# Performance work log

Measured on AMD Instinct MI355X. Metric: run time of the kernel, lower is better.

The kernel has to match this reference:

```python
import jax, jax.numpy as jnp
import numpy as np

N, C, E = 10000, 128, 640000  # nodes, channels, edges


def setup_inputs() -> dict:
    key = jax.random.key(0)
    k1, k2, k3, k4 = jax.random.split(key, 4)
    x = jax.random.normal(k1, (N, C), dtype=jnp.float32)
    src = jax.random.randint(k2, (E,), 0, N)  # source node of each edge (neighbor j)
    dst = jax.random.randint(k3, (E,), 0, N)  # destination node (center i)
    # EdgeConv linear: in = 2*C (concat[x_i, x_j - x_i]), out = C
    W = jax.random.normal(k4, (2 * C, C), dtype=jnp.float32) / np.sqrt(2.0 * C)
    b = jnp.zeros((C,), dtype=jnp.float32)
    return {"x": x, "W": W, "b": b, "src": src, "dst": dst}


def reference(x, W, b, src, dst):
    # EdgeConv: h_i = max_{j in N(i)} Linear([x_i, x_j - x_i]); then ReLU
    xi = x[dst]                                   # [E, C] gather center feats
    xj = x[src]                                   # [E, C] gather neighbor feats
    msg = jnp.concatenate([xi, xj - xi], axis=-1) @ W + b   # [E, C]
    agg = jax.ops.segment_max(msg, dst, num_segments=x.shape[0])  # [N, C]
    # nodes with no incoming edges get -inf from segment_max; zero them
    agg = jnp.where(jnp.isfinite(agg), agg, jnp.zeros_like(agg))
    return jax.nn.relu(agg)
```

## Files before the change

### kernel.cpp

```cpp
#include <hip/hip_runtime.h>
#include <cstdint>


#define C_CH 128
#define NBLK 128
#define NMAX_LDS 10016

typedef __attribute__((ext_vector_type(8))) short bf16x8;
typedef __attribute__((ext_vector_type(4))) float f32x4;
typedef __attribute__((ext_vector_type(4))) unsigned int u32x4;

static inline size_t align_up(size_t v, size_t a) { return (v + a - 1) & ~(a - 1); }

__device__ inline unsigned f2bf_bits(float f) {
    unsigned u = __builtin_bit_cast(unsigned, f);
    return (u + 0x7FFFu + ((u >> 16) & 1u)) >> 16;
}

__global__ __launch_bounds__(256) void gemm_mfma(const float* __restrict__ x,
                                                 const float* __restrict__ W,
                                                 const float* __restrict__ bias,
                                                 float* __restrict__ Aarr,
                                                 unsigned short* __restrict__ Bbf,
                                                 int Nn) {
    __shared__ unsigned short Wh[64][136];
    __shared__ unsigned short Wl[64][136];
    int tid = threadIdx.x;
    int col0 = blockIdx.y * 64;
    bool isA = (col0 < C_CH);
    for (int idx = tid; idx < 64 * 64; idx += 256) {
        int c = idx & 63, k = (idx >> 6) * 2;
        int gc = col0 + c;
        float w0, w1;
        if (isA) {
            w0 = W[k * C_CH + gc] - W[(k + C_CH) * C_CH + gc];
            w1 = W[(k + 1) * C_CH + gc] - W[(k + 1 + C_CH) * C_CH + gc];
        } else {
            int g2 = gc - C_CH;
            w0 = W[(k + C_CH) * C_CH + g2];
            w1 = W[(k + 1 + C_CH) * C_CH + g2];
        }
        unsigned h0 = f2bf_bits(w0), h1 = f2bf_bits(w1);
        float hf0 = __builtin_bit_cast(float, h0 << 16);
        float hf1 = __builtin_bit_cast(float, h1 << 16);
        unsigned l0 = f2bf_bits(w0 - hf0), l1 = f2bf_bits(w1 - hf1);
        *(unsigned*)&Wh[c][k] = h0 | (h1 << 16);
        *(unsigned*)&Wl[c][k] = l0 | (l1 << 16);
    }
    __syncthreads();
    int lane = tid & 63, wv = tid >> 6;
    int r0 = blockIdx.x * 64 + wv * 16;
    int arow = min(r0 + (lane & 15), Nn - 1);
    int kgrp = (lane >> 4) * 8;
    f32x4 acc[4] = {};
#pragma unroll
    for (int kk = 0; kk < 4; ++kk) {
        int k0 = kk * 32 + kgrp;
        const float* xp = &x[(size_t)arow * C_CH + k0];
        float4 v0 = *(const float4*)xp;
        float4 v1 = *(const float4*)(xp + 4);
        float vv[8] = {v0.x, v0.y, v0.z, v0.w, v1.x, v1.y, v1.z, v1.w};
        bf16x8 ah, al;
#pragma unroll
        for (int u = 0; u < 8; ++u) {
            unsigned hb = f2bf_bits(vv[u]);
            float hf = __builtin_bit_cast(float, hb << 16);
            ah[u] = (short)hb;
            al[u] = (short)f2bf_bits(vv[u] - hf);
        }
#pragma unroll
        for (int j = 0; j < 4; ++j) {
            int c = j * 16 + (lane & 15);
            bf16x8 bh = *(const bf16x8*)&Wh[c][k0];
            bf16x8 bl = *(const bf16x8*)&Wl[c][k0];
            acc[j] = __builtin_amdgcn_mfma_f32_16x16x32_bf16(ah, bh, acc[j], 0, 0, 0);
            acc[j] = __builtin_amdgcn_mfma_f32_16x16x32_bf16(al, bh, acc[j], 0, 0, 0);
            acc[j] = __builtin_amdgcn_mfma_f32_16x16x32_bf16(ah, bl, acc[j], 0, 0, 0);
        }
    }
#pragma unroll
    for (int j = 0; j < 4; ++j) {
        int gc = col0 + j * 16 + (lane & 15);
        float badd = isA ? bias[gc] : 0.f;
#pragma unroll
        for (int reg = 0; reg < 4; ++reg) {
            int row = r0 + (lane >> 4) * 4 + reg;
            if (row < Nn) {
                if (isA) Aarr[(size_t)row * C_CH + gc] = acc[j][reg] + badd;
                else     Bbf[(size_t)row * C_CH + (gc - C_CH)] =
                             (unsigned short)f2bf_bits(acc[j][reg]);
            }
        }
    }
}

__global__ __launch_bounds__(256) void hist_k(const int* __restrict__ dst,
                                              int* __restrict__ T,
                                              int E_, int Nn, int chunk) {
    __shared__ int ldeg[NMAX_LDS];
    int tid = threadIdx.x, b = blockIdx.x;
    for (int i = tid; i < Nn; i += 256) ldeg[i] = 0;
    __syncthreads();
    int e0 = b * chunk, e1 = min(e0 + chunk, E_);
    int n4 = (e1 - e0) >> 2;
    const int4* d4p = (const int4*)(dst + e0);
    for (int i = tid; i < n4; i += 256) {
        int4 d = d4p[i];
        atomicAdd(&ldeg[d.x], 1); atomicAdd(&ldeg[d.y], 1);
        atomicAdd(&ldeg[d.z], 1); atomicAdd(&ldeg[d.w], 1);
    }
    for (int i = e0 + n4 * 4 + tid; i < e1; i += 256) atomicAdd(&ldeg[dst[i]], 1);
    __syncthreads();
    int* Tb = T + (size_t)b * Nn;
    for (int i = tid; i < Nn; i += 256) Tb[i] = ldeg[i];
}

__global__ __launch_bounds__(256) void colscan_k(int* __restrict__ T,
                                                 int* __restrict__ deg, int Nn) {
    int tid = threadIdx.x;
    int lane = tid & 63;
    int n = blockIdx.x * 4 + (tid >> 6);
    if (n >= Nn) return;
    size_t st = (size_t)Nn;
    int e0 = T[lane * st + n];
    int e1 = T[(lane + 64) * st + n];
    int i0 = e0, i1 = e1;
#pragma unroll
    for (int off = 1; off < 64; off <<= 1) {
        int t0 = __shfl_up(i0, off);
        int t1 = __shfl_up(i1, off);
        if (lane >= off) { i0 += t0; i1 += t1; }
    }
    int tot0 = __shfl(i0, 63);
    int tot1 = __shfl(i1, 63);
    T[lane * st + n] = i0 - e0;
    T[(lane + 64) * st + n] = tot0 + i1 - e1;
    if (lane == 0) deg[n] = tot0 + tot1;
}

__global__ __launch_bounds__(1024) void scan_k(const int* __restrict__ deg,
                                               int* __restrict__ offs, int n) {
    __shared__ int wsum[16];
    const int PER = 16;
    int tid = threadIdx.x;
    int base = tid * PER;
    int s = 0;
#pragma unroll
    for (int k = 0; k < PER; ++k) {
        int idx = base + k;
        s += (idx < n) ? deg[idx] : 0;
    }
    int lane = tid & 63, wid = tid >> 6;
    int pref = s;
#pragma unroll
    for (int off = 1; off < 64; off <<= 1) {
        int t = __shfl_up(pref, off);
        if (lane >= off) pref += t;
    }
    if (lane == 63) wsum[wid] = pref;
    __syncthreads();
    if (tid < 16) {
        int v = wsum[tid];
#pragma unroll
        for (int off = 1; off < 16; off <<= 1) {
            int t = __shfl_up(v, off, 16);
            if (tid >= off) v += t;
        }
        wsum[tid] = v;
    }
    __syncthreads();
    int run = ((wid > 0) ? wsum[wid - 1] : 0) + (pref - s);
#pragma unroll
    for (int k = 0; k < PER; ++k) {
        int idx = base + k;
        int v = (idx < n) ? deg[idx] : 0;
        if (idx < n) offs[idx] = run;
        run += v;
    }
    if (tid == 1023) offs[n] = run;
}

__global__ __launch_bounds__(256) void scatter_k(const int* __restrict__ src,
                                                 const int* __restrict__ dst,
                                                 const int* __restrict__ T,
                                                 const int* __restrict__ offs,
                                                 int* __restrict__ ssrc,
                                                 int E_, int Nn, int chunk) {
    __shared__ int sbase[NMAX_LDS];
    __shared__ int ldeg[NMAX_LDS];
    int tid = threadIdx.x, b = blockIdx.x;
    const int* Tb = T + (size_t)b * Nn;
    for (int i = tid; i < Nn; i += 256) {
        sbase[i] = offs[i] + Tb[i];
        ldeg[i] = 0;
    }
    __syncthreads();
    int e0 = b * chunk, e1 = min(e0 + chunk, E_);
    int n4 = (e1 - e0) >> 2;
    const int4* d4p = (const int4*)(dst + e0);
    const int4* s4p = (const int4*)(src + e0);
    for (int i = tid; i < n4; i += 256) {
        int4 d = d4p[i];
        int4 sv = s4p[i];
        int r;
        r = atomicAdd(&ldeg[d.x], 1); ssrc[sbase[d.x] + r] = sv.x;
        r = atomicAdd(&ldeg[d.y], 1); ssrc[sbase[d.y] + r] = sv.y;
        r = atomicAdd(&ldeg[d.z], 1); ssrc[sbase[d.z] + r] = sv.z;
        r = atomicAdd(&ldeg[d.w], 1); ssrc[sbase[d.w] + r] = sv.w;
    }
    for (int i = e0 + n4 * 4 + tid; i < e1; i += 256) {
        int d = dst[i];
        int r = atomicAdd(&ldeg[d], 1);
        ssrc[sbase[d] + r] = src[i];
    }
}

__global__ __launch_bounds__(256) void node_max(const float* __restrict__ Aarr,
                                                const unsigned short* __restrict__ Bbf,
                                                const int* __restrict__ offs,
                                                const int* __restrict__ ssrc,
                                                float* __restrict__ out, int Nn) {
    int i = blockIdx.x;
    int tid = threadIdx.x;
    int s = offs[i], e = offs[i + 1];
    if (e == s) {
        if (tid < 32) ((float4*)out)[(size_t)i * 32 + tid] = make_float4(0.f, 0.f, 0.f, 0.f);
        return;
    }
    __shared__ int js[256];
    __shared__ float pm[4][16][8];
    int g = tid >> 4;
    int l16 = tid & 15;
    int cb = l16 * 8;
    float m[8];
#pragma unroll
    for (int k = 0; k < 8; ++k) m[k] = -INFINITY;
    for (int base = s; base < e; base += 256) {
        __syncthreads();
        js[tid] = ssrc[min(base + tid, e - 1)];
        __syncthreads();
        int cnt = min(256, e - base);
        for (int t = g; t < cnt; t += 64) {
            u32x4 v[4];
#pragma unroll
            for (int u = 0; u < 4; ++u) {
                int idx = min(t + 16 * u, cnt - 1);
                v[u] = *(const u32x4*)&Bbf[(size_t)js[idx] * C_CH + cb];
            }
#pragma unroll
            for (int u = 0; u < 4; ++u) {
#pragma unroll
                for (int p = 0; p < 4; ++p) {
                    unsigned w = v[u][p];
                    float f0 = __builtin_bit_cast(float, w << 16);
                    float f1 = __builtin_bit_cast(float, w & 0xFFFF0000u);
                    m[2 * p]     = fmaxf(m[2 * p], f0);
                    m[2 * p + 1] = fmaxf(m[2 * p + 1], f1);
                }
            }
        }
    }
#pragma unroll
    for (int k = 0; k < 8; ++k) {
        m[k] = fmaxf(m[k], __shfl_xor(m[k], 16));
        m[k] = fmaxf(m[k], __shfl_xor(m[k], 32));
    }
    __syncthreads();
    int wid = tid >> 6;
    if ((tid & 63) < 16) {
#pragma unroll
        for (int k = 0; k < 8; ++k) pm[wid][l16][k] = m[k];
    }
    __syncthreads();
    if (tid < C_CH) {
        int c = tid;
        float mm = fmaxf(fmaxf(pm[0][c >> 3][c & 7], pm[1][c >> 3][c & 7]),
                         fmaxf(pm[2][c >> 3][c & 7], pm[3][c >> 3][c & 7]));
        float a = Aarr[(size_t)i * C_CH + c];
        out[(size_t)i * C_CH + c] = fmaxf(a + mm, 0.f);
    }
}

extern "C" void kernel_launch(void* const* d_in, const int* in_sizes, int n_in,
                              void* d_out, int out_size, void* d_ws, size_t ws_size,
                              hipStream_t stream) {
    const float* x = (const float*)d_in[0];
    const float* W = (const float*)d_in[1];
    const float* b = (const float*)d_in[2];
    const int* src = (const int*)d_in[3];
    const int* dst = (const int*)d_in[4];
    float* out = (float*)d_out;

    const int N = in_sizes[0] / C_CH;
    const int E = in_sizes[3];
    const int chunk = (((E + NBLK - 1) / NBLK) + 3) & ~3;

    char* w = (char*)d_ws;
    float* Aarr = (float*)w;            w += align_up((size_t)N * C_CH * 4, 256);
    unsigned short* Bbf = (unsigned short*)w;  w += align_up((size_t)N * C_CH * 2, 256);
    int* deg = (int*)w;                 w += align_up((size_t)N * 4, 256);
    int* offs = (int*)w;                w += align_up((size_t)(N + 1) * 4, 256);
    int* T = (int*)w;                   w += align_up((size_t)NBLK * N * 4, 256);
    int* ssrc = (int*)w;                w += align_up((size_t)E * 4, 256);

    gemm_mfma<<<dim3((N + 63) / 64, 4), 256, 0, stream>>>(x, W, b, Aarr, Bbf, N);
    hist_k<<<NBLK, 256, 0, stream>>>(dst, T, E, N, chunk);
    colscan_k<<<(N + 3) / 4, 256, 0, stream>>>(T, deg, N);
    scan_k<<<1, 1024, 0, stream>>>(deg, offs, N);
    scatter_k<<<NBLK, 256, 0, stream>>>(src, dst, T, offs, ssrc, E, N, chunk);
    node_max<<<N, 256, 0, stream>>>(Aarr, Bbf, offs, ssrc, out, N);
}
```

Baseline: 147.5 us.

## Bucket edges by groups of 16 destinations and reduce with LDS atomicMax

Replaces the per-node CSR sort with a coarse counting sort into buckets of 16 destination nodes, storing the packed (src, local dst) pair per edge. This shrinks the histogram and scan tables (640 buckets instead of 10000 nodes) and uses 256 blocks. A new bucket_max kernel gives one 512-thread block per bucket and accumulates per-channel maxima in LDS through monotonic-key atomicMax. The cost is that each edge now reads its bf16 row with scalar 2-byte loads and does LDS atomics per channel, instead of the previous vectorised register max reduction.

```diff
diff --git a/kernel.cpp b/kernel.cpp
--- a/kernel.cpp
+++ b/kernel.cpp
@@ -3,18 +3,21 @@
 
 
 #define C_CH 128
-#define NBLK 128
-#define NMAX_LDS 10016
+#define HBLK 256
+#define BSH 4
+#define BPAD 640
 
 typedef __attribute__((ext_vector_type(8))) short bf16x8;
 typedef __attribute__((ext_vector_type(4))) float f32x4;
-typedef __attribute__((ext_vector_type(4))) unsigned int u32x4;
 
 static inline size_t align_up(size_t v, size_t a) { return (v + a - 1) & ~(a - 1); }
 
 __device__ inline unsigned f2bf_bits(float f) {
     unsigned u = __builtin_bit_cast(unsigned, f);
     return (u + 0x7FFFu + ((u >> 16) & 1u)) >> 16;
+}
+__device__ inline unsigned mono_key(unsigned u) {
+    return (u & 0x80000000u) ? ~u : (u | 0x80000000u);
 }
 
 __global__ __launch_bounds__(256) void gemm_mfma(const float* __restrict__ x,
@@ -94,48 +97,49 @@
     }
 }
 
-__global__ __launch_bounds__(256) void hist_k(const int* __restrict__ dst,
-                                              int* __restrict__ T,
-                                              int E_, int Nn, int chunk) {
-    __shared__ int ldeg[NMAX_LDS];
+__global__ __launch_bounds__(256) void hist2_k(const int* __restrict__ dst,
+                                               int* __restrict__ T2,
+                                               int E_, int NBq, int chunk) {
+    __shared__ int cnt[BPAD];
     int tid = threadIdx.x, b = blockIdx.x;
-    for (int i = tid; i < Nn; i += 256) ldeg[i] = 0;
+    for (int i = tid; i < BPAD; i += 256) cnt[i] = 0;
     __syncthreads();
     int e0 = b * chunk, e1 = min(e0 + chunk, E_);
     int n4 = (e1 - e0) >> 2;
     const int4* d4p = (const int4*)(dst + e0);
     for (int i = tid; i < n4; i += 256) {
         int4 d = d4p[i];
-        atomicAdd(&ldeg[d.x], 1); atomicAdd(&ldeg[d.y], 1);
-        atomicAdd(&ldeg[d.z], 1); atomicAdd(&ldeg[d.w], 1);
-    }
-    for (int i = e0 + n4 * 4 + tid; i < e1; i += 256) atomicAdd(&ldeg[dst[i]], 1);
-    __syncthreads();
-    int* Tb = T + (size_t)b * Nn;
-    for (int i = tid; i < Nn; i += 256) Tb[i] = ldeg[i];
-}
-
-__global__ __launch_bounds__(256) void colscan_k(int* __restrict__ T,
-                                                 int* __restrict__ deg, int Nn) {
+        atomicAdd(&cnt[d.x >> BSH], 1); atomicAdd(&cnt[d.y >> BSH], 1);
+        atomicAdd(&cnt[d.z >> BSH], 1); atomicAdd(&cnt[d.w >> BSH], 1);
+    }
+    for (int i = e0 + n4 * 4 + tid; i < e1; i += 256) atomicAdd(&cnt[dst[i] >> BSH], 1);
+    __syncthreads();
+    int* Tb = T2 + (size_t)b * BPAD;
+    for (int i = tid; i < NBq; i += 256) Tb[i] = cnt[i];
+}
+
+__global__ __launch_bounds__(256) void colscan2_k(int* __restrict__ T2,
+                                                  int* __restrict__ deg2, int NBq) {
     int tid = threadIdx.x;
     int lane = tid & 63;
-    int n = blockIdx.x * 4 + (tid >> 6);
-    if (n >= Nn) return;
-    size_t st = (size_t)Nn;
-    int e0 = T[lane * st + n];
-    int e1 = T[(lane + 64) * st + n];
-    int i0 = e0, i1 = e1;
+    int q = blockIdx.x * 4 + (tid >> 6);
+    if (q >= NBq) return;
+    int e[4], p[4];
+#pragma unroll
+    for (int k = 0; k < 4; ++k) e[k] = T2[(size_t)(lane + 64 * k) * BPAD + q];
+    int s = 0;
+#pragma unroll
+    for (int k = 0; k < 4; ++k) { p[k] = s; s += e[k]; }
+    int incl = s;
 #pragma unroll
     for (int off = 1; off < 64; off <<= 1) {
-        int t0 = __shfl_up(i0, off);
-        int t1 = __shfl_up(i1, off);
-        if (lane >= off) { i0 += t0; i1 += t1; }
-    }
-    int tot0 = __shfl(i0, 63);
-    int tot1 = __shfl(i1, 63);
-    T[lane * st + n] = i0 - e0;
-    T[(lane + 64) * st + n] = tot0 + i1 - e1;
-    if (lane == 0) deg[n] = tot0 + tot1;
+        int t = __shfl_up(incl, off);
+        if (lane >= off) incl += t;
+    }
+    int excl = incl - s;
+#pragma unroll
+    for (int k = 0; k < 4; ++k) T2[(size_t)(lane + 64 * k) * BPAD + q] = excl + p[k];
+    if (lane == 63) deg2[q] = incl;
 }
 
 __global__ __launch_bounds__(1024) void scan_k(const int* __restrict__ deg,
@@ -180,104 +184,93 @@
     if (tid == 1023) offs[n] = run;
 }
 
-__global__ __launch_bounds__(256) void scatter_k(const int* __restrict__ src,
-                                                 const int* __restrict__ dst,
-                                                 const int* __restrict__ T,
-                                                 const int* __restrict__ offs,
-                                                 int* __restrict__ ssrc,
-                                                 int E_, int Nn, int chunk) {
-    __shared__ int sbase[NMAX_LDS];
-    __shared__ int ldeg[NMAX_LDS];
+__global__ __launch_bounds__(256) void scatter2_k(const int* __restrict__ src,
+                                                  const int* __restrict__ dst,
+                                                  const int* __restrict__ T2,
+                                                  const int* __restrict__ offs2,
+                                                  unsigned* __restrict__ epack,
+                                                  int E_, int NBq, int chunk) {
+    __shared__ int sbase[BPAD];
+    __shared__ int cur[BPAD];
     int tid = threadIdx.x, b = blockIdx.x;
-    const int* Tb = T + (size_t)b * Nn;
-    for (int i = tid; i < Nn; i += 256) {
-        sbase[i] = offs[i] + Tb[i];
-        ldeg[i] = 0;
+    const int* Tb = T2 + (size_t)b * BPAD;
+    for (int i = tid; i < NBq; i += 256) {
+        sbase[i] = offs2[i] + Tb[i];
+        cur[i] = 0;
     }
     __syncthreads();
     int e0 = b * chunk, e1 = min(e0 + chunk, E_);
     int n4 = (e1 - e0) >> 2;
     const int4* d4p = (const int4*)(dst + e0);
     const int4* s4p = (const int4*)(src + e0);
+    const int LM = (1 << BSH) - 1;
     for (int i = tid; i < n4; i += 256) {
         int4 d = d4p[i];
         int4 sv = s4p[i];
-        int r;
-        r = atomicAdd(&ldeg[d.x], 1); ssrc[sbase[d.x] + r] = sv.x;
-        r = atomicAdd(&ldeg[d.y], 1); ssrc[sbase[d.y] + r] = sv.y;
-        r = atomicAdd(&ldeg[d.z], 1); ssrc[sbase[d.z] + r] = sv.z;
-        r = atomicAdd(&ldeg[d.w], 1); ssrc[sbase[d.w] + r] = sv.w;
+        int q, r;
+        q = d.x >> BSH; r = atomicAdd(&cur[q], 1);
+        epack[sbase[q] + r] = ((unsigned)sv.x << BSH) | (unsigned)(d.x & LM);
+        q = d.y >> BSH; r = atomicAdd(&cur[q], 1);
+        epack[sbase[q] + r] = ((unsigned)sv.y << BSH) | (unsigned)(d.y & LM);
+        q = d.z >> BSH; r = atomicAdd(&cur[q], 1);
+        epack[sbase[q] + r] = ((unsigned)sv.z << BSH) | (unsigned)(d.z & LM);
+        q = d.w >> BSH; r = atomicAdd(&cur[q], 1);
+        epack[sbase[q] + r] = ((unsigned)sv.w << BSH) | (unsigned)(d.w & LM);
     }
     for (int i = e0 + n4 * 4 + tid; i < e1; i += 256) {
         int d = dst[i];
-        int r = atomicAdd(&ldeg[d], 1);
-        ssrc[sbase[d] + r] = src[i];
-    }
-}
-
-__global__ __launch_bounds__(256) void node_max(const float* __restrict__ Aarr,
-                                                const unsigned short* __restrict__ Bbf,
-                                                const int* __restrict__ offs,
-                                                const int* __restrict__ ssrc,
-                                                float* __restrict__ out, int Nn) {
-    int i = blockIdx.x;
+        int q = d >> BSH;
+        int r = atomicAdd(&cur[q], 1);
+        epack[sbase[q] + r] = ((unsigned)src[i] << BSH) | (unsigned)(d & LM);
+    }
+}
+
+__global__ __launch_bounds__(512) void bucket_max(const float* __restrict__ Aarr,
+                                                  const unsigned short* __restrict__ Bbf,
+                                                  const int* __restrict__ offs2,
+                                                  const unsigned* __restrict__ epack,
+                                                  float* __restrict__ out, int Nn) {
+    int q = blockIdx.x;
+    int n0 = q << BSH;
+    if (n0 >= Nn) return;
+    __shared__ unsigned acc[1 << BSH][C_CH];
     int tid = threadIdx.x;
-    int s = offs[i], e = offs[i + 1];
-    if (e == s) {
-        if (tid < 32) ((float4*)out)[(size_t)i * 32 + tid] = make_float4(0.f, 0.f, 0.f, 0.f);
-        return;
-    }
-    __shared__ int js[256];
-    __shared__ float pm[4][16][8];
-    int g = tid >> 4;
-    int l16 = tid & 15;
-    int cb = l16 * 8;
-    float m[8];
-#pragma unroll
-    for (int k = 0; k < 8; ++k) m[k] = -INFINITY;
-    for (int base = s; base < e; base += 256) {
-        __syncthreads();
-        js[tid] = ssrc[min(base + tid, e - 1)];
-        __syncthreads();
-        int cnt = min(256, e - base);
-        for (int t = g; t < cnt; t += 64) {
-            u32x4 v[4];
-#pragma unroll
-            for (int u = 0; u < 4; ++u) {
-                int idx = min(t + 16 * u, cnt - 1);
-                v[u] = *(const u32x4*)&Bbf[(size_t)js[idx] * C_CH + cb];
+    int nloc = min(1 << BSH, Nn - n0);
+    for (int i = tid; i < (1 << BSH) * C_CH; i += 512) ((unsigned*)acc)[i] = 0u;
+    __syncthreads();
+    int s = offs2[q], e = offs2[q + 1];
+    int lane = tid & 63, w = tid >> 6;
+    const int LM = (1 << BSH) - 1;
+    for (int g0 = s + w * 64; g0 < e; g0 += 512) {
+        int idx = g0 + lane;
+        unsigned pk = (idx < e) ? epack[idx] : 0u;
+        int cnt = min(64, e - g0);
+#pragma unroll 4
+        for (int j = 0; j < cnt; ++j) {
+            unsigned p = __shfl(pk, j);
+            const unsigned short* bp = &Bbf[(size_t)(p >> BSH) * C_CH];
+            unsigned loc = p & LM;
+            unsigned k0 = mono_key(((unsigned)bp[lane]) << 16);
+            unsigned k1 = mono_key(((unsigned)bp[lane + 64]) << 16);
+            atomicMax(&acc[loc][lane], k0);
+            atomicMax(&acc[loc][lane + 64], k1);
+        }
+    }
+    __syncthreads();
+    for (int p0 = 0; p0 < nloc; p0 += 4) {
+        int li = p0 + (tid >> 7);
+        int c = tid & 127;
+        if (li < nloc) {
+            int row = n0 + li;
+            unsigned key = acc[li][c];
+            float v = 0.f;
+            if (key != 0u) {
+                unsigned u = (key & 0x80000000u) ? (key & 0x7FFFFFFFu) : ~key;
+                float bmax = __builtin_bit_cast(float, u);
+                v = fmaxf(Aarr[(size_t)row * C_CH + c] + bmax, 0.f);
             }
-#pragma unroll
-            for (int u = 0; u < 4; ++u) {
-#pragma unroll
-                for (int p = 0; p < 4; ++p) {
-                    unsigned w = v[u][p];
-                    float f0 = __builtin_bit_cast(float, w << 16);
-                    float f1 = __builtin_bit_cast(float, w & 0xFFFF0000u);
-                    m[2 * p]     = fmaxf(m[2 * p], f0);
-                    m[2 * p + 1] = fmaxf(m[2 * p + 1], f1);
-                }
-            }
-        }
-    }
-#pragma unroll
-    for (int k = 0; k < 8; ++k) {
-        m[k] = fmaxf(m[k], __shfl_xor(m[k], 16));
-        m[k] = fmaxf(m[k], __shfl_xor(m[k], 32));
-    }
-    __syncthreads();
-    int wid = tid >> 6;
-    if ((tid & 63) < 16) {
-#pragma unroll
-        for (int k = 0; k < 8; ++k) pm[wid][l16][k] = m[k];
-    }
-    __syncthreads();
-    if (tid < C_CH) {
-        int c = tid;
-        float mm = fmaxf(fmaxf(pm[0][c >> 3][c & 7], pm[1][c >> 3][c & 7]),
-                         fmaxf(pm[2][c >> 3][c & 7], pm[3][c >> 3][c & 7]));
-        float a = Aarr[(size_t)i * C_CH + c];
-        out[(size_t)i * C_CH + c] = fmaxf(a + mm, 0.f);
+            out[(size_t)row * C_CH + c] = v;
+        }
     }
 }
 
@@ -293,20 +286,21 @@
 
     const int N = in_sizes[0] / C_CH;
     const int E = in_sizes[3];
-    const int chunk = (((E + NBLK - 1) / NBLK) + 3) & ~3;
+    const int NBq = (N + (1 << BSH) - 1) >> BSH;
+    const int chunk = (((E + HBLK - 1) / HBLK) + 3) & ~3;
 
     char* w = (char*)d_ws;
-    float* Aarr = (float*)w;            w += align_up((size_t)N * C_CH * 4, 256);
+    float* Aarr = (float*)w;                   w += align_up((size_t)N * C_CH * 4, 256);
     unsigned short* Bbf = (unsigned short*)w;  w += align_up((size_t)N * C_CH * 2, 256);
-    int* deg = (int*)w;                 w += align_up((size_t)N * 4, 256);
-    int* offs = (int*)w;                w += align_up((size_t)(N + 1) * 4, 256);
-    int* T = (int*)w;                   w += align_up((size_t)NBLK * N * 4, 256);
-    int* ssrc = (int*)w;                w += align_up((size_t)E * 4, 256);
+    int* deg2 = (int*)w;                       w += align_up((size_t)BPAD * 4, 256);
+    int* offs2 = (int*)w;                      w += align_up((size_t)(BPAD + 1) * 4, 256);
+    int* T2 = (int*)w;                         w += align_up((size_t)HBLK * BPAD * 4, 256);
+    unsigned* epack = (unsigned*)w;            w += align_up((size_t)E * 4, 256);
 
     gemm_mfma<<<dim3((N + 63) / 64, 4), 256, 0, stream>>>(x, W, b, Aarr, Bbf, N);
-    hist_k<<<NBLK, 256, 0, stream>>>(dst, T, E, N, chunk);
-    colscan_k<<<(N + 3) / 4, 256, 0, stream>>>(T, deg, N);
-    scan_k<<<1, 1024, 0, stream>>>(deg, offs, N);
-    scatter_k<<<NBLK, 256, 0, stream>>>(src, dst, T, offs, ssrc, E, N, chunk);
-    node_max<<<N, 256, 0, stream>>>(Aarr, Bbf, offs, ssrc, out, N);
-}
+    hist2_k<<<HBLK, 256, 0, stream>>>(dst, T2, E, NBq, chunk);
+    colscan2_k<<<(NBq + 3) / 4, 256, 0, stream>>>(T2, deg2, NBq);
+    scan_k<<<1, 1024, 0, stream>>>(deg2, offs2, NBq);
+    scatter2_k<<<HBLK, 256, 0, stream>>>(src, dst, T2, offs2, epack, E, NBq, chunk);
+    bucket_max<<<NBq, 512, 0, stream>>>(Aarr, Bbf, offs2, epack, out, N);
+}
```

Result: no change. 147.9 us (+0.2%).
